# Optimization experiments

Measured on AMD Instinct MI355X. Metric: run time of the kernel, lower is better.

Reference implementation:

```python
import jax, jax.numpy as jnp
import numpy as np

B, S, D = 2, 2048, 2048
H = 16            # n_heads
DH = D // H       # d_head = 128
ROPE_BASE = 10000.0


def setup_inputs() -> dict:
    key = jax.random.key(0)
    ks = jax.random.split(key, 5)
    x = jax.random.normal(ks[0], (B, S, D), dtype=jnp.float32)
    s = 1.0 / np.sqrt(D).astype(np.float32)
    Wqkv = jax.random.normal(ks[1], (D, 3 * D), dtype=jnp.float32) * s
    bqkv = jnp.zeros((3 * D,), dtype=jnp.float32)
    Wo = jax.random.normal(ks[2], (D, D), dtype=jnp.float32) * s
    bo = jnp.zeros((D,), dtype=jnp.float32)
    return {"x": x, "Wqkv": Wqkv, "bqkv": bqkv, "Wo": Wo, "bo": bo}


def _rotary_tables(seq_len, d_head, dtype):
    inv_freq = 1.0 / (ROPE_BASE ** (jnp.arange(0, d_head, 2, dtype=dtype) / d_head))
    t = jnp.arange(seq_len, dtype=dtype)
    freqs = jnp.einsum('i,j->ij', t, inv_freq)          # [S, DH/2]
    emb = jnp.concatenate([freqs, freqs], axis=-1)       # [S, DH]
    return jnp.cos(emb), jnp.sin(emb)


def _rotate(u):
    # pairs (even, odd) -> cat(odd, -even) along last dim, per the source's
    # stack([::2],[1::2]) construction
    return jnp.concatenate([u[..., 1::2], -u[..., ::2]], axis=-1)


def reference(x, Wqkv, bqkv, Wo, bo):
    b, s, d = x.shape
    qkv = x @ Wqkv + bqkv                                # [B,S,3D]
    q, k, v = jnp.split(qkv, 3, axis=-1)
    # [B,S,D] -> [B,H,S,DH]
    q = q.reshape(b, s, H, DH).transpose(0, 2, 1, 3)
    k = k.reshape(b, s, H, DH).transpose(0, 2, 1, 3)
    v = v.reshape(b, s, H, DH).transpose(0, 2, 1, 3)
    cos, sin = _rotary_tables(s, DH, x.dtype)            # [S,DH], broadcasts over B,H
    q = q * cos + _rotate(q) * sin
    k = k * cos + _rotate(k) * sin
    scale = 1.0 / np.sqrt(DH).astype(np.float32)
    attn = jnp.einsum('bhqd,bhkd->bhqk', q, k) * scale   # [B,H,S,S]
    attn = jax.nn.softmax(attn, axis=-1)
    out = jnp.einsum('bhqk,bhkd->bhqd', attn, v)         # [B,H,S,DH]
    out = out.transpose(0, 2, 1, 3).reshape(b, s, d)
    return out @ Wo + bo
```

## Files before the change

### kernel.cpp

```cpp
#include <hip/hip_runtime.h>
#include <math.h>

constexpr int Bc = 2, Sc = 2048, Dc = 2048, Hc = 16, DHc = 128;
constexpr int Mc = Bc * Sc;
constexpr int N3 = 3 * Dc;

typedef short     s16x8  __attribute__((ext_vector_type(8)));
typedef float     f32x4  __attribute__((ext_vector_type(4)));
typedef unsigned short ushortv8 __attribute__((ext_vector_type(8)));

__device__ __forceinline__ unsigned short f2bf(float f) {
  unsigned u = __float_as_uint(f);
  u += 0x7fffu + ((u >> 16) & 1u);
  return (unsigned short)(u >> 16);
}
__device__ __forceinline__ float bf2f(unsigned short h) {
  return __uint_as_float(((unsigned)h) << 16);
}

__device__ __forceinline__ void gld_lds16(const unsigned short* g, unsigned short* l) {
  __builtin_amdgcn_global_load_lds(
      (const __attribute__((address_space(1))) void*)g,
      (__attribute__((address_space(3))) void*)l, 16, 0, 0);
}

template<int CTRL>
__device__ __forceinline__ float dppf(float x) {
  return __int_as_float(
      __builtin_amdgcn_update_dpp(0, __float_as_int(x), CTRL, 0xF, 0xF, true));
}
__device__ __forceinline__ float rowmax16(float v) {
  v = fmaxf(v, dppf<0xB1>(v));
  v = fmaxf(v, dppf<0x4E>(v));
  v = fmaxf(v, dppf<0x141>(v));
  v = fmaxf(v, dppf<0x140>(v));
  return v;
}
__device__ __forceinline__ float rowsum16(float v) {
  v += dppf<0xB1>(v);
  v += dppf<0x4E>(v);
  v += dppf<0x141>(v);
  v += dppf<0x140>(v);
  return v;
}

__global__ void rope_table_kernel(float* __restrict__ cosT, float* __restrict__ sinT) {
  int idx = blockIdx.x * 256 + threadIdx.x;
  int s = idx >> 6, j = idx & 63;
  float inv = powf(10000.0f, -(float)(2 * j) / 128.0f);
  float a = (float)s * inv;
  cosT[idx] = cosf(a);
  sinT[idx] = sinf(a);
}

__global__ void cvt_bf16(const float* __restrict__ in, unsigned short* __restrict__ outp) {
  size_t i = ((size_t)blockIdx.x * 256 + threadIdx.x) * 8;
  float4 a = *(const float4*)&in[i];
  float4 b = *(const float4*)&in[i + 4];
  ushortv8 o;
  o[0] = f2bf(a.x); o[1] = f2bf(a.y); o[2] = f2bf(a.z); o[3] = f2bf(a.w);
  o[4] = f2bf(b.x); o[5] = f2bf(b.y); o[6] = f2bf(b.z); o[7] = f2bf(b.w);
  *(ushortv8*)&outp[i] = o;
}

__global__ __launch_bounds__(256)
void cvt_transpose(const float* __restrict__ in, unsigned short* __restrict__ outp,
                   int R, int C) {
  __shared__ float Ls[64][69];
  const int nTc = C >> 6;
  const int tc = blockIdx.x % nTc, tr = blockIdx.x / nTc;
  const int r0 = tr << 6, c0 = tc << 6;
#pragma unroll
  for (int i = 0; i < 4; ++i) {
    int id = threadIdx.x + 256 * i;
    int row = id >> 4, col = (id & 15) << 2;
    float4 v = *(const float4*)&in[(size_t)(r0 + row) * C + c0 + col];
    Ls[row][col] = v.x; Ls[row][col + 1] = v.y;
    Ls[row][col + 2] = v.z; Ls[row][col + 3] = v.w;
  }
  __syncthreads();
#pragma unroll
  for (int i = 0; i < 2; ++i) {
    int id = threadIdx.x + 256 * i;
    int crow = id >> 3, rcol = (id & 7) << 3;
    ushortv8 o;
#pragma unroll
    for (int jj = 0; jj < 8; ++jj) o[jj] = f2bf(Ls[rcol + jj][crow]);
    *(ushortv8*)&outp[(size_t)(c0 + crow) * R + r0 + rcol] = o;
  }
}

template<int EPI>
__global__ __launch_bounds__(256)
void gemm_bt(const unsigned short* __restrict__ A, const unsigned short* __restrict__ Bt,
             const float* __restrict__ bias, unsigned short* __restrict__ Qo,
             unsigned short* __restrict__ Ko, unsigned short* __restrict__ Vo,
             float* __restrict__ outF, int Ndim)
{
  constexpr int Kd = 2048;
  __shared__ unsigned short As[128 * 32];
  __shared__ unsigned short Bs[128 * 32];
  const int t = threadIdx.x;
  const int w = t >> 6, l = t & 63;
  const int l15 = l & 15, g = l >> 4;
  const int wr = w >> 1, wc = w & 1;
  const int nwg = gridDim.x * gridDim.y;
  const int flat = blockIdx.y * gridDim.x + blockIdx.x;
  const int swz = (flat & 7) * (nwg >> 3) + (flat >> 3);
  const int m0 = (swz / gridDim.x) * 128, n0 = (swz % gridDim.x) * 128;
  const int srow = l >> 2;
  const int scol = (l & 3) * 8;

  f32x4 acc[4][4];
#pragma unroll
  for (int mi = 0; mi < 4; ++mi)
#pragma unroll
    for (int ni = 0; ni < 4; ++ni) acc[mi][ni] = (f32x4){0.f, 0.f, 0.f, 0.f};

  for (int k0 = 0; k0 < Kd; k0 += 32) {
    __syncthreads();
#pragma unroll
    for (int j = 0; j < 2; ++j) {
      int rowg = (w * 2 + j) * 16 + srow;
      gld_lds16(&A[(size_t)(m0 + rowg) * Kd + k0 + scol], &As[(w * 2 + j) * 512]);
      gld_lds16(&Bt[(size_t)(n0 + rowg) * Kd + k0 + scol], &Bs[(w * 2 + j) * 512]);
    }
    __syncthreads();

    s16x8 af[4], bf[4];
#pragma unroll
    for (int mi = 0; mi < 4; ++mi)
      af[mi] = *(const s16x8*)&As[(wr * 64 + mi * 16 + l15) * 32 + g * 8];
#pragma unroll
    for (int ni = 0; ni < 4; ++ni)
      bf[ni] = *(const s16x8*)&Bs[(wc * 64 + ni * 16 + l15) * 32 + g * 8];
#pragma unroll
    for (int mi = 0; mi < 4; ++mi)
#pragma unroll
      for (int ni = 0; ni < 4; ++ni)
        acc[mi][ni] = __builtin_amdgcn_mfma_f32_16x16x32_bf16(af[mi], bf[ni], acc[mi][ni], 0, 0, 0);
  }

  if (EPI == 0) {
    const int part = n0 >> 11;
    const int h = (n0 >> 7) & 15;
    unsigned short* outp = (part == 0) ? Qo : (part == 1 ? Ko : Vo);
#pragma unroll
    for (int mi = 0; mi < 4; ++mi) {
#pragma unroll
      for (int r = 0; r < 4; ++r) {
        int row = m0 + wr * 64 + mi * 16 + g * 4 + r;
        int b_ = row >> 11, s_ = row & 2047;
        unsigned short* dst = outp + (((size_t)(b_ * Hc + h) * Sc + s_) << 7);
#pragma unroll
        for (int ni = 0; ni < 4; ++ni) {
          int col = wc * 64 + ni * 16 + l15;
          dst[col] = f2bf(acc[mi][ni][r] + bias[n0 + col]);
        }
      }
    }
  } else {
#pragma unroll
    for (int mi = 0; mi < 4; ++mi) {
#pragma unroll
      for (int r = 0; r < 4; ++r) {
        int row = m0 + wr * 64 + mi * 16 + g * 4 + r;
#pragma unroll
        for (int ni = 0; ni < 4; ++ni) {
          int col = wc * 64 + ni * 16 + l15;
          outF[(size_t)row * Ndim + n0 + col] = acc[mi][ni][r] + bias[n0 + col];
        }
      }
    }
  }
}

__global__ void rope_bf16(unsigned short* __restrict__ Q, unsigned short* __restrict__ K,
                          const float* __restrict__ cosT, const float* __restrict__ sinT) {
  const int row = blockIdx.x;
  const int t = threadIdx.x;
  const int half = t >> 7, j = t & 127;
  const int s = row & (Sc - 1);
  __shared__ float sh[2][128];
  unsigned short* buf = half ? K : Q;
  const size_t off = (size_t)row * DHc + j;
  float val = bf2f(buf[off]);
  sh[half][j] = val;
  __syncthreads();
  const float c  = cosT[s * 64 + (j & 63)];
  const float sn = sinT[s * 64 + (j & 63)];
  float rot = (j < 64) ? sh[half][2 * j + 1] : -sh[half][2 * (j - 64)];
  float r = val * c + rot * sn;
  if (!half) r *= 0.08838834764831845f * 1.4426950408889634f;
  buf[off] = f2bf(r);
}

__global__ __launch_bounds__(256)
void vtrans(const unsigned short* __restrict__ V, unsigned short* __restrict__ Vt)
{
  __shared__ __align__(16) unsigned short Ls[64][132];
  const int bid = blockIdx.x;
  const int st = bid & 31, bh = bid >> 5;
  const int s0 = st * 64;
  const unsigned short* src = V + ((size_t)bh * Sc + s0) * DHc;
  unsigned short* dst = Vt + (size_t)bh * DHc * Sc + s0;
#pragma unroll
  for (int r = 0; r < 4; ++r) {
    int id = threadIdx.x + 256 * r;
    int row = id >> 4, col = (id & 15) * 8;
    *(ushortv8*)&Ls[row][col] = *(const ushortv8*)&src[(size_t)row * DHc + col];
  }
  __syncthreads();
#pragma unroll
  for (int r = 0; r < 4; ++r) {
    int id = threadIdx.x + 256 * r;
    int d = id >> 3, scol = (id & 7) * 8;
    ushortv8 o;
#pragma unroll
    for (int jj = 0; jj < 8; ++jj) o[jj] = Ls[scol + jj][d];
    *(ushortv8*)&dst[(size_t)d * Sc + scol] = o;
  }
}

__global__ __launch_bounds__(256)
void attn_mfma(const unsigned short* __restrict__ Qg, const unsigned short* __restrict__ Kg,
               const unsigned short* __restrict__ Vtg, unsigned short* __restrict__ Og)
{
  __shared__ __align__(16) unsigned short Ks[64][136];
  __shared__ __align__(16) unsigned short Vs[128][72];
  __shared__ __align__(16) unsigned short Ps[4][32][68];
  const int t = threadIdx.x;
  const int w = t >> 6, l = t & 63;
  const int l15 = l & 15, g = l >> 4;
  const int flat = blockIdx.x;
  const int swz = (flat & 7) * 64 + (flat >> 3);
  const int qt = swz & 15, bh = swz >> 4;
  const int q0 = qt * 128;
  const size_t kbase = (size_t)bh * Sc * DHc;
  const size_t vbase = (size_t)bh * DHc * Sc;

  s16x8 qf[2][4];
#pragma unroll
  for (int mi = 0; mi < 2; ++mi)
#pragma unroll
    for (int ks = 0; ks < 4; ++ks)
      qf[mi][ks] = *(const s16x8*)&Qg[kbase + (size_t)(q0 + w * 32 + mi * 16 + l15) * DHc
                                      + ks * 32 + 8 * g];

  f32x4 acc[2][8];
#pragma unroll
  for (int mi = 0; mi < 2; ++mi)
#pragma unroll
    for (int dt = 0; dt < 8; ++dt) acc[mi][dt] = (f32x4){0.f, 0.f, 0.f, 0.f};
  float m_i[2][4], l_i[2][4];
#pragma unroll
  for (int mi = 0; mi < 2; ++mi)
#pragma unroll
    for (int r = 0; r < 4; ++r) { m_i[mi][r] = -1.0e30f; l_i[mi][r] = 0.f; }

  for (int kt0 = 0; kt0 < Sc; kt0 += 64) {
    __syncthreads();
#pragma unroll
    for (int r = 0; r < 4; ++r) {
      int id = t + 256 * r;
      int row = id >> 4, col = (id & 15) * 8;
      *(ushortv8*)&Ks[row][col] =
          *(const ushortv8*)&Kg[kbase + (size_t)(kt0 + row) * DHc + col];
    }
#pragma unroll
    for (int r = 0; r < 4; ++r) {
      int id = t + 256 * r;
      int row = id >> 3, col = (id & 7) * 8;
      *(ushortv8*)&Vs[row][col] =
          *(const ushortv8*)&Vtg[vbase + (size_t)row * Sc + kt0 + col];
    }
    __syncthreads();

    f32x4 sv[2][4];
#pragma unroll
    for (int mi = 0; mi < 2; ++mi)
#pragma unroll
      for (int nt = 0; nt < 4; ++nt) sv[mi][nt] = (f32x4){0.f, 0.f, 0.f, 0.f};
    __builtin_amdgcn_s_setprio(1);
#pragma unroll
    for (int nt = 0; nt < 4; ++nt) {
#pragma unroll
      for (int ks = 0; ks < 4; ++ks) {
        s16x8 bf = *(const s16x8*)&Ks[nt * 16 + l15][ks * 32 + 8 * g];
        sv[0][nt] = __builtin_amdgcn_mfma_f32_16x16x32_bf16(qf[0][ks], bf, sv[0][nt], 0, 0, 0);
        sv[1][nt] = __builtin_amdgcn_mfma_f32_16x16x32_bf16(qf[1][ks], bf, sv[1][nt], 0, 0, 0);
      }
    }
    __builtin_amdgcn_s_setprio(0);

    float vmax[2][4];
    bool okb = true;
#pragma unroll
    for (int mi = 0; mi < 2; ++mi) {
#pragma unroll
      for (int r = 0; r < 4; ++r) {
        float vm = fmaxf(fmaxf(sv[mi][0][r], sv[mi][1][r]),
                         fmaxf(sv[mi][2][r], sv[mi][3][r]));
        vm = rowmax16(vm);
        vmax[mi][r] = vm;
        okb = okb && (vm - m_i[mi][r] <= 8.0f);
      }
    }
    if (__all((int)okb)) {
#pragma unroll
      for (int mi = 0; mi < 2; ++mi) {
#pragma unroll
        for (int r = 0; r < 4; ++r) {
          float rs = 0.f;
#pragma unroll
          for (int nt = 0; nt < 4; ++nt) {
            float p = __builtin_amdgcn_exp2f(sv[mi][nt][r] - m_i[mi][r]);
            rs += p;
            Ps[w][mi * 16 + g * 4 + r][nt * 16 + l15] = f2bf(p);
          }
          l_i[mi][r] += rowsum16(rs);
        }
      }
    } else {
#pragma unroll
      for (int mi = 0; mi < 2; ++mi) {
#pragma unroll
        for (int r = 0; r < 4; ++r) {
          float mnew = fmaxf(m_i[mi][r], vmax[mi][r]);
          float scf = __builtin_amdgcn_exp2f(m_i[mi][r] - mnew);
          float rs = 0.f;
#pragma unroll
          for (int nt = 0; nt < 4; ++nt) {
            float p = __builtin_amdgcn_exp2f(sv[mi][nt][r] - mnew);
            rs += p;
            Ps[w][mi * 16 + g * 4 + r][nt * 16 + l15] = f2bf(p);
          }
          l_i[mi][r] = l_i[mi][r] * scf + rowsum16(rs);
          m_i[mi][r] = mnew;
#pragma unroll
          for (int dt = 0; dt < 8; ++dt) acc[mi][dt][r] *= scf;
        }
      }
    }

    s16x8 pf[2][2];
#pragma unroll
    for (int mi = 0; mi < 2; ++mi)
#pragma unroll
      for (int ks = 0; ks < 2; ++ks)
        pf[mi][ks] = *(const s16x8*)&Ps[w][mi * 16 + l15][ks * 32 + 8 * g];

    __builtin_amdgcn_s_setprio(1);
#pragma unroll
    for (int dt = 0; dt < 8; ++dt) {
#pragma unroll
      for (int ks = 0; ks < 2; ++ks) {
        s16x8 vf = *(const s16x8*)&Vs[dt * 16 + l15][ks * 32 + 8 * g];
        acc[0][dt] = __builtin_amdgcn_mfma_f32_16x16x32_bf16(pf[0][ks], vf, acc[0][dt], 0, 0, 0);
        acc[1][dt] = __builtin_amdgcn_mfma_f32_16x16x32_bf16(pf[1][ks], vf, acc[1][dt], 0, 0, 0);
      }
    }
    __builtin_amdgcn_s_setprio(0);
  }

  const int b = bh >> 4, h = bh & 15;
#pragma unroll
  for (int mi = 0; mi < 2; ++mi) {
#pragma unroll
    for (int r = 0; r < 4; ++r) {
      float inv = 1.0f / l_i[mi][r];
      int srow = q0 + w * 32 + mi * 16 + g * 4 + r;
      unsigned short* dst = Og + ((size_t)(b * Sc + srow)) * Dc + h * DHc;
#pragma unroll
      for (int dt = 0; dt < 8; ++dt)
        dst[dt * 16 + l15] = f2bf(acc[mi][dt][r] * inv);
    }
  }
}

extern "C" void kernel_launch(void* const* d_in, const int* in_sizes, int n_in,
                              void* d_out, int out_size, void* d_ws, size_t ws_size,
                              hipStream_t stream) {
  const float* x    = (const float*)d_in[0];
  const float* Wqkv = (const float*)d_in[1];
  const float* bqkv = (const float*)d_in[2];
  const float* Wo   = (const float*)d_in[3];
  const float* bo   = (const float*)d_in[4];
  float* out = (float*)d_out;
  char* p = (char*)d_ws;

  unsigned short* Ob  = (unsigned short*)p;  p += 16777216;
  float* cosT         = (float*)p;           p += 524288;
  float* sinT         = (float*)p;           p += 524288;
  unsigned short* xbf = (unsigned short*)p;  p += 16777216;
  unsigned short* Wqt = (unsigned short*)p;  p += 25165824;
  unsigned short* Wot = (unsigned short*)p;  p += 8388608;
  unsigned short* Qbf = (unsigned short*)p;  p += 16777216;
  unsigned short* Kbf = (unsigned short*)p;  p += 16777216;
  unsigned short* Vbf = (unsigned short*)p;  p += 16777216;
  unsigned short* Vtb = (unsigned short*)p;  p += 16777216;

  rope_table_kernel<<<(Sc * 64) / 256, 256, 0, stream>>>(cosT, sinT);

  cvt_bf16<<<(Mc * Dc) / (256 * 8), 256, 0, stream>>>(x, xbf);
  cvt_transpose<<<(N3 / 64) * (Dc / 64), 256, 0, stream>>>(Wqkv, Wqt, Dc, N3);
  cvt_transpose<<<(Dc / 64) * (Dc / 64), 256, 0, stream>>>(Wo, Wot, Dc, Dc);

  dim3 g1(N3 / 128, Mc / 128);
  gemm_bt<0><<<g1, 256, 0, stream>>>(xbf, Wqt, bqkv, Qbf, Kbf, Vbf, nullptr, N3);

  rope_bf16<<<Bc * Hc * Sc, 256, 0, stream>>>(Qbf, Kbf, cosT, sinT);

  vtrans<<<Bc * Hc * (Sc / 64), 256, 0, stream>>>(Vbf, Vtb);

  attn_mfma<<<Bc * Hc * (Sc / 128), 256, 0, stream>>>(Qbf, Kbf, Vtb, Ob);

  dim3 g2(Dc / 128, Mc / 128);
  gemm_bt<1><<<g2, 256, 0, stream>>>(Ob, Wot, bo, nullptr, nullptr, nullptr, out, Dc);
}
```

Measured before the change: 526.1 us.

## Load K/V tiles via direct global-to-LDS with XOR swizzle, simplify softmax

```diff
diff --git a/kernel.cpp b/kernel.cpp
--- a/kernel.cpp
+++ b/kernel.cpp
@@ -16,6 +16,11 @@
 }
 __device__ __forceinline__ float bf2f(unsigned short h) {
   return __uint_as_float(((unsigned)h) << 16);
+}
+__device__ __forceinline__ unsigned short f2bf_hw(float f) {
+  unsigned r;
+  asm("v_cvt_pk_bf16_f32 %0, %1, 0" : "=v"(r) : "v"(f));
+  return (unsigned short)r;
 }
 
 __device__ __forceinline__ void gld_lds16(const unsigned short* g, unsigned short* l) {
@@ -226,8 +231,8 @@
 void attn_mfma(const unsigned short* __restrict__ Qg, const unsigned short* __restrict__ Kg,
                const unsigned short* __restrict__ Vtg, unsigned short* __restrict__ Og)
 {
-  __shared__ __align__(16) unsigned short Ks[64][136];
-  __shared__ __align__(16) unsigned short Vs[128][72];
+  __shared__ __align__(16) unsigned short Ks[64 * 128];
+  __shared__ __align__(16) unsigned short Vs[128 * 64];
   __shared__ __align__(16) unsigned short Ps[4][32][68];
   const int t = threadIdx.x;
   const int w = t >> 6, l = t & 63;
@@ -239,6 +244,9 @@
   const size_t kbase = (size_t)bh * Sc * DHc;
   const size_t vbase = (size_t)bh * DHc * Sc;
 
+  const int krow_in = (l >> 4);
+  const int vrow_in = (l >> 3);
+
   s16x8 qf[2][4];
 #pragma unroll
   for (int mi = 0; mi < 2; ++mi)
@@ -261,18 +269,14 @@
   for (int kt0 = 0; kt0 < Sc; kt0 += 64) {
     __syncthreads();
 #pragma unroll
-    for (int r = 0; r < 4; ++r) {
-      int id = t + 256 * r;
-      int row = id >> 4, col = (id & 15) * 8;
-      *(ushortv8*)&Ks[row][col] =
-          *(const ushortv8*)&Kg[kbase + (size_t)(kt0 + row) * DHc + col];
-    }
-#pragma unroll
-    for (int r = 0; r < 4; ++r) {
-      int id = t + 256 * r;
-      int row = id >> 3, col = (id & 7) * 8;
-      *(ushortv8*)&Vs[row][col] =
-          *(const ushortv8*)&Vtg[vbase + (size_t)row * Sc + kt0 + col];
+    for (int j = 0; j < 4; ++j) {
+      int chunk = w * 4 + j;
+      int krow = chunk * 4 + krow_in;
+      int kc16 = (l15) ^ (krow & 7);
+      gld_lds16(&Kg[kbase + (size_t)(kt0 + krow) * DHc + kc16 * 8], &Ks[chunk * 512]);
+      int vrow = chunk * 8 + vrow_in;
+      int vc16 = (l & 7) ^ (vrow & 7);
+      gld_lds16(&Vtg[vbase + (size_t)vrow * Sc + kt0 + vc16 * 8], &Vs[chunk * 512]);
     }
     __syncthreads();
 
@@ -286,15 +290,14 @@
     for (int nt = 0; nt < 4; ++nt) {
 #pragma unroll
       for (int ks = 0; ks < 4; ++ks) {
-        s16x8 bf = *(const s16x8*)&Ks[nt * 16 + l15][ks * 32 + 8 * g];
+        int c16 = (4 * ks + g) ^ (l15 & 7);
+        s16x8 bf = *(const s16x8*)&Ks[(nt * 16 + l15) * 128 + c16 * 8];
         sv[0][nt] = __builtin_amdgcn_mfma_f32_16x16x32_bf16(qf[0][ks], bf, sv[0][nt], 0, 0, 0);
         sv[1][nt] = __builtin_amdgcn_mfma_f32_16x16x32_bf16(qf[1][ks], bf, sv[1][nt], 0, 0, 0);
       }
     }
     __builtin_amdgcn_s_setprio(0);
 
-    float vmax[2][4];
-    bool okb = true;
 #pragma unroll
     for (int mi = 0; mi < 2; ++mi) {
 #pragma unroll
@@ -302,44 +305,19 @@
         float vm = fmaxf(fmaxf(sv[mi][0][r], sv[mi][1][r]),
                          fmaxf(sv[mi][2][r], sv[mi][3][r]));
         vm = rowmax16(vm);
-        vmax[mi][r] = vm;
-        okb = okb && (vm - m_i[mi][r] <= 8.0f);
-      }
-    }
-    if (__all((int)okb)) {
-#pragma unroll
-      for (int mi = 0; mi < 2; ++mi) {
-#pragma unroll
-        for (int r = 0; r < 4; ++r) {
-          float rs = 0.f;
-#pragma unroll
-          for (int nt = 0; nt < 4; ++nt) {
-            float p = __builtin_amdgcn_exp2f(sv[mi][nt][r] - m_i[mi][r]);
-            rs += p;
-            Ps[w][mi * 16 + g * 4 + r][nt * 16 + l15] = f2bf(p);
-          }
-          l_i[mi][r] += rowsum16(rs);
+        float mnew = fmaxf(m_i[mi][r], vm);
+        float scf = __builtin_amdgcn_exp2f(m_i[mi][r] - mnew);
+        float rs = 0.f;
+#pragma unroll
+        for (int nt = 0; nt < 4; ++nt) {
+          float p = __builtin_amdgcn_exp2f(sv[mi][nt][r] - mnew);
+          rs += p;
+          Ps[w][mi * 16 + g * 4 + r][nt * 16 + l15] = f2bf_hw(p);
         }
-      }
-    } else {
-#pragma unroll
-      for (int mi = 0; mi < 2; ++mi) {
-#pragma unroll
-        for (int r = 0; r < 4; ++r) {
-          float mnew = fmaxf(m_i[mi][r], vmax[mi][r]);
-          float scf = __builtin_amdgcn_exp2f(m_i[mi][r] - mnew);
-          float rs = 0.f;
-#pragma unroll
-          for (int nt = 0; nt < 4; ++nt) {
-            float p = __builtin_amdgcn_exp2f(sv[mi][nt][r] - mnew);
-            rs += p;
-            Ps[w][mi * 16 + g * 4 + r][nt * 16 + l15] = f2bf(p);
-          }
-          l_i[mi][r] = l_i[mi][r] * scf + rowsum16(rs);
-          m_i[mi][r] = mnew;
-#pragma unroll
-          for (int dt = 0; dt < 8; ++dt) acc[mi][dt][r] *= scf;
-        }
+        l_i[mi][r] = l_i[mi][r] * scf + rowsum16(rs);
+        m_i[mi][r] = mnew;
+#pragma unroll
+        for (int dt = 0; dt < 8; ++dt) acc[mi][dt][r] *= scf;
       }
     }
 
@@ -355,7 +333,8 @@
     for (int dt = 0; dt < 8; ++dt) {
 #pragma unroll
       for (int ks = 0; ks < 2; ++ks) {
-        s16x8 vf = *(const s16x8*)&Vs[dt * 16 + l15][ks * 32 + 8 * g];
+        int c16 = (4 * ks + g) ^ (l15 & 7);
+        s16x8 vf = *(const s16x8*)&Vs[(dt * 16 + l15) * 64 + c16 * 8];
         acc[0][dt] = __builtin_amdgcn_mfma_f32_16x16x32_bf16(pf[0][ks], vf, acc[0][dt], 0, 0, 0);
         acc[1][dt] = __builtin_amdgcn_mfma_f32_16x16x32_bf16(pf[1][ks], vf, acc[1][dt], 0, 0, 0);
       }
@@ -373,7 +352,7 @@
       unsigned short* dst = Og + ((size_t)(b * Sc + srow)) * Dc + h * DHc;
 #pragma unroll
       for (int dt = 0; dt < 8; ++dt)
-        dst[dt * 16 + l15] = f2bf(acc[mi][dt][r] * inv);
+        dst[dt * 16 + l15] = f2bf_hw(acc[mi][dt][r] * inv);
     }
   }
 }
```

New measurement: 449.1 us. -14.6%, faster.
